# Kernel tuning notes

Hardware: AMD Instinct MI355X
Metric: run time of the kernel (lower is better)

The kernel has to match this reference:

```python
import jax, jax.numpy as jnp
import numpy as np

DIM = 1024
HEAD_DIM = 64
NUM_HEADS = DIM // HEAD_DIM
SCALE = HEAD_DIM ** -0.5
B, N, M = 2, 1024, 2048


def setup_inputs() -> dict:
    key = jax.random.key(0)
    ks = jax.random.split(key, 7)
    x = jax.random.normal(ks[0], (B, N, DIM), dtype=jnp.float32)
    context = jax.random.normal(ks[1], (B, M, DIM), dtype=jnp.float32)
    # query row has at least one valid key (avoids all -inf softmax rows).
    mask = jax.random.bernoulli(ks[2], 0.9, (B, N, M))
    mask = mask.at[:, :, 0].set(True)
    # Linear params (torch nn.Linear convention: y = x @ W.T + b)
    sq = (1.0 / DIM) ** 0.5
    Wq = jax.random.uniform(ks[3], (DIM, DIM), minval=-sq, maxval=sq, dtype=jnp.float32)
    Wkv = jax.random.uniform(ks[4], (2 * DIM, DIM), minval=-sq, maxval=sq, dtype=jnp.float32)
    b_kv = jax.random.uniform(ks[5], (2 * DIM,), minval=-sq, maxval=sq, dtype=jnp.float32)
    Wo = jax.random.uniform(ks[6], (DIM, DIM), minval=-sq, maxval=sq, dtype=jnp.float32)
    return {"x": x, "context": context, "mask": mask,
            "Wq": Wq, "Wkv": Wkv, "b_kv": b_kv, "Wo": Wo}


def reference(x, context, mask, Wq, Wkv, b_kv, Wo):
    b, n, c = x.shape
    m = context.shape[1]
    h, d = NUM_HEADS, HEAD_DIM
    # Q projection (no bias): [b, n, h, d] -> bhnd
    q = (x @ Wq.T).reshape(b, n, h, d).transpose(0, 2, 1, 3)
    # KV projection (with bias): [b, m, 2, h, d]
    kv = (context @ Wkv.T + b_kv).reshape(b, m, 2, h, d)
    k = kv[:, :, 0].transpose(0, 2, 1, 3)  # bhmd
    v = kv[:, :, 1].transpose(0, 2, 1, 3)  # bhmd
    # scores: bhnm, scale applied after matmul as in the original
    attn = jnp.einsum('bhnd,bhmd->bhnm', q, k) * SCALE
    attn = jnp.where(mask[:, None, :, :], attn, -jnp.inf)
    attn = jax.nn.softmax(attn, axis=-1)
    out = jnp.einsum('bhnm,bhmd->bhnd', attn, v)
    out = out.transpose(0, 2, 1, 3).reshape(b, n, h * d)
    return out @ Wo.T
```

## Files before the change

### kernel.cpp

```cpp
#include <hip/hip_runtime.h>


typedef __attribute__((ext_vector_type(8))) short short8;
typedef __attribute__((ext_vector_type(4))) short short4v;
typedef __attribute__((ext_vector_type(4))) float f32x4;

#define SCL2E 0.18033688011112042592f

__device__ __forceinline__ float bf2f(short s) {
  unsigned u = ((unsigned)(unsigned short)s) << 16;
  return __uint_as_float(u);
}
__device__ __forceinline__ short f2bf(float f) {
  unsigned u = __float_as_uint(f);
  u += 0x7fffu + ((u >> 16) & 1u);
  return (short)(u >> 16);
}
__device__ __forceinline__ void gld_lds16(const void* gp, void* lp) {
  __builtin_amdgcn_global_load_lds(
      (const __attribute__((address_space(1))) unsigned int*)gp,
      (__attribute__((address_space(3))) unsigned int*)lp, 16, 0, 0);
}
__device__ __forceinline__ short4v cvt4(float4 v) {
  short4v o;
  o[0] = f2bf(v.x); o[1] = f2bf(v.y); o[2] = f2bf(v.z); o[3] = f2bf(v.w);
  return o;
}
__device__ __forceinline__ size_t off128(int row, int k) {
  return ((size_t)(((row >> 7) * 32 + (k >> 5)) * 8 + ((row >> 4) & 7)) << 9) +
         (((((k >> 3) & 3) * 16 + (row & 15)) << 3) + (k & 7));
}
__device__ __forceinline__ size_t off64(int row, int k) {
  return ((size_t)(((row >> 6) * 32 + (k >> 5)) * 4 + ((row >> 4) & 3)) << 9) +
         (((((k >> 3) & 3) * 16 + (row & 15)) << 3) + (k & 7));
}

__global__ __launch_bounds__(256) void prep(
    const unsigned char* __restrict__ mask, unsigned long long* __restrict__ pm,
    const float* __restrict__ Wq, const float* __restrict__ Wkv,
    const float* __restrict__ Wo, const float* __restrict__ x,
    const float* __restrict__ ctx, short* __restrict__ wqb,
    short* __restrict__ wkvb, short* __restrict__ wob,
    short* __restrict__ xb, short* __restrict__ ctxb) {
  const int row = blockIdx.x;
  const int wave = threadIdx.x >> 6, lane = threadIdx.x & 63;
  const unsigned char p8 = mask[lane * 4 + 1];
  const int p32 = ((const int*)mask)[lane * 2 + 1];
  const int shift =
      (__ballot(p8 != 0) != 0ull) ? 0 : ((__ballot(p32 != 0) != 0ull) ? 2 : 3);
  const size_t mbase = ((size_t)row * 2048) << shift;
#pragma unroll
  for (int j = 0; j < 8; j++) {
    const int c = wave * 512 + j * 64 + lane;
    const unsigned long long bits = __ballot(mask[mbase + ((size_t)c << shift)] != 0);
    if (lane == 0) pm[(size_t)row * 32 + wave * 8 + j] = bits;
  }
  const int gid = blockIdx.x * 256 + threadIdx.x;
  {
    const int e = gid * 4, r = e >> 10, k = e & 1023;
    *(short4v*)(xb + off128(r, k)) = cvt4(((const float4*)x)[gid]);
  }
  {
    int e = gid * 4, r = e >> 10, k = e & 1023;
    *(short4v*)(ctxb + off128(r, k)) = cvt4(((const float4*)ctx)[gid]);
    e = (gid + 524288) * 4; r = e >> 10; k = e & 1023;
    *(short4v*)(ctxb + off128(r, k)) = cvt4(((const float4*)ctx)[gid + 524288]);
  }
  {
    const int e = gid * 4, r = e >> 10, k = e & 1023;
    *(short4v*)(wkvb + off128(r, k)) = cvt4(((const float4*)Wkv)[gid]);
  }
  if (gid < 262144) {
    const int e = gid * 4, r = e >> 10, k = e & 1023;
    *(short4v*)(wqb + off128(r, k)) = cvt4(((const float4*)Wq)[gid]);
    *(short4v*)(wob + off64(r, k)) = cvt4(((const float4*)Wo)[gid]);
  }
}

__global__ __launch_bounds__(256, 2)
void qkv_gemm(const short* __restrict__ xb, const short* __restrict__ ctxb,
              const short* __restrict__ wqb, const short* __restrict__ wkvb,
              const float* __restrict__ bias, short* __restrict__ qws,
              short* __restrict__ kws, short* __restrict__ vtws) {
  __shared__ __align__(16) short ldsA[8 * 512];
  __shared__ __align__(16) short ldsB[8 * 512];
  const int tid = threadIdx.x;
  const int wave = tid >> 6, lane = tid & 63;
  const int l15 = lane & 15, lg = lane >> 4;
  const int bx = blockIdx.x;
  const bool isKV = bx < 512;
  const int rt = isKV ? (bx >> 4) : ((bx - 512) >> 3);
  const int ct = isKV ? (bx & 15) : ((bx - 512) & 7);
  const short* Amat = isKV ? ctxb : xb;
  const short* Bw = isKV ? wkvb : wqb;
  const int wr = wave >> 1, wc = wave & 1;

  f32x4 acc[4][4];
#pragma unroll
  for (int i = 0; i < 4; i++)
#pragma unroll
    for (int j = 0; j < 4; j++) acc[i][j] = (f32x4){0.f, 0.f, 0.f, 0.f};

  const short* ga0 = Amat + (size_t)rt * 131072 + wave * 512 + lane * 8;
  const short* ga1 = ga0 + 2048;
  const short* gb0 = Bw + (size_t)ct * 131072 + wave * 512 + lane * 8;
  const short* gb1 = gb0 + 2048;
  short* la0 = &ldsA[wave * 512];
  short* la1 = &ldsA[(wave + 4) * 512];
  short* lb0 = &ldsB[wave * 512];
  short* lb1 = &ldsB[(wave + 4) * 512];

  for (int k0 = 0; k0 < 1024; k0 += 32) {
    const size_t koff = (size_t)(k0 >> 5) * 4096;
    __syncthreads();
    gld_lds16(ga0 + koff, la0);
    gld_lds16(ga1 + koff, la1);
    gld_lds16(gb0 + koff, lb0);
    gld_lds16(gb1 + koff, lb1);
    __syncthreads();
    short8 af[4], bfr[4];
#pragma unroll
    for (int t = 0; t < 4; t++)
      af[t] = *(const short8*)&ldsA[((wr * 4 + t) * 64 + lane) * 8];
#pragma unroll
    for (int t = 0; t < 4; t++)
      bfr[t] = *(const short8*)&ldsB[((wc * 4 + t) * 64 + lane) * 8];
#pragma unroll
    for (int i = 0; i < 4; i++)
#pragma unroll
      for (int j = 0; j < 4; j++)
        acc[i][j] =
            __builtin_amdgcn_mfma_f32_16x16x32_bf16(af[i], bfr[j], acc[i][j], 0, 0, 0);
  }

#pragma unroll
  for (int i = 0; i < 4; i++)
#pragma unroll
    for (int j = 0; j < 4; j++)
#pragma unroll
      for (int r = 0; r < 4; r++) {
        const int gr = rt * 128 + wr * 64 + i * 16 + lg * 4 + r;
        const int gc = ct * 128 + wc * 64 + j * 16 + l15;
        float v = acc[i][j][r];
        if (isKV) {
          v += bias[gc];
          const int b = gr >> 11, m = gr & 2047;
          const int kv = gc >> 10, hh = (gc >> 6) & 15, d = gc & 63;
          if (kv == 0)
            kws[((((size_t)b * 16 + hh) * 2048 + m) << 6) + d] = f2bf(v);
          else
            vtws[(((size_t)b * 16 + hh) * 64 + d) * 2048 + m] = f2bf(v);
        } else {
          const int b = gr >> 10, n = gr & 1023, hh = gc >> 6, d = gc & 63;
          qws[((((size_t)b * 16 + hh) * 1024 + n) << 6) + d] = f2bf(v * SCL2E);
        }
      }
}

__global__ __launch_bounds__(512, 2)
void attn_split(const short* __restrict__ Qg, const short* __restrict__ Kg,
                const short* __restrict__ Vtg,
                const unsigned int* __restrict__ pm,
                float* __restrict__ opart, float* __restrict__ lpart) {
  __shared__ __align__(16) short ldsK[8192];
  __shared__ __align__(16) short ldsV[8192];
  __shared__ __align__(16) short ldsP[17408];
  __shared__ __align__(16) short ones[512];
  const int tid = threadIdx.x;
  const int w = tid >> 6, lane = tid & 63;
  const int l15 = lane & 15, lg = lane >> 4;
  const int bx = blockIdx.x;
  const int bhid = bx & 31, qt = (bx >> 5) & 7, half = bx >> 8;
  const int b = bhid >> 4, h = bhid & 15;
  const int n0 = qt * 128, m_base = half * 1024;
  const size_t bh = (size_t)b * 16 + h;
  const short* Qb = Qg + (bh * 1024 + n0) * 64;
  const short* Kb = Kg + (bh << 17);
  const short* Vb = Vtg + (bh << 17);
  const unsigned int* pmw =
      pm + ((size_t)(b * 1024 + n0 + w * 16 + lg * 4) << 6) + (m_base >> 5);

  ones[tid] = 0x3F80;
#pragma unroll
  for (int ii = 0; ii < 2; ii++)
    gld_lds16(Qb + (size_t)(w * 16 + l15) * 64 + ii * 32 + lg * 8,
              &ldsP[(w * 2 + ii) * 512]);
  __syncthreads();
  short8 qf[2];
#pragma unroll
  for (int ks = 0; ks < 2; ks++)
    qf[ks] = *(const short8*)&ldsP[((w * 2 + ks) * 64 + lane) * 8];
  const short8 onesf = *(const short8*)&ones[lane * 8];

  f32x4 o[4], lacc;
#pragma unroll
  for (int ct = 0; ct < 4; ct++) o[ct] = (f32x4){0.f, 0.f, 0.f, 0.f};
  lacc = (f32x4){0.f, 0.f, 0.f, 0.f};
  short* Pme = &ldsP[w * 2176];

  uint4 mk[4], mkn[4];
#pragma unroll
  for (int r = 0; r < 4; r++) mk[r] = *(const uint4*)(pmw + (size_t)r * 64);

  for (int c = 0; c < 8; c++) {
    const int m0 = m_base + c * 128;
    __syncthreads();
#pragma unroll
    for (int ii = 0; ii < 2; ii++) {
      const int f = w * 2 + ii;
      const int t = f >> 1, ks = f & 1;
      gld_lds16(Kb + (size_t)(m0 + t * 16 + l15) * 64 + ks * 32 + lg * 8,
                &ldsK[f * 512]);
      const int ct = f >> 2, ks2 = f & 3;
      gld_lds16(Vb + (size_t)(ct * 16 + l15) * 2048 + (m0 + ks2 * 32 + lg * 8),
                &ldsV[f * 512]);
    }
    if (c < 7) {
#pragma unroll
      for (int r = 0; r < 4; r++)
        mkn[r] = *(const uint4*)(pmw + (size_t)r * 64 + (c + 1) * 4);
    }
    __syncthreads();

    f32x4 s[8];
#pragma unroll
    for (int t = 0; t < 8; t++) s[t] = (f32x4){0.f, 0.f, 0.f, 0.f};
#pragma unroll
    for (int t = 0; t < 8; t++)
#pragma unroll
      for (int ks = 0; ks < 2; ks++) {
        short8 kf = *(const short8*)&ldsK[((t * 2 + ks) * 64 + lane) * 8];
        s[t] = __builtin_amdgcn_mfma_f32_16x16x32_bf16(qf[ks], kf, s[t], 0, 0, 0);
      }

#pragma unroll
    for (int r = 0; r < 4; r++) {
      const unsigned int* mwp = (const unsigned int*)&mk[r];
#pragma unroll
      for (int t = 0; t < 8; t++) {
        const bool att = (mwp[t >> 1] >> (((t & 1) << 4) + l15)) & 1;
        const float p = exp2f(att ? s[t][r] : -1e30f);
        Pme[(lg * 4 + r) * 136 + t * 16 + l15] = f2bf(p);
      }
    }
    short8 pf[4];
#pragma unroll
    for (int ks2 = 0; ks2 < 4; ks2++)
      pf[ks2] = *(const short8*)&Pme[l15 * 136 + ks2 * 32 + lg * 8];
#pragma unroll
    for (int ct = 0; ct < 4; ct++)
#pragma unroll
      for (int ks2 = 0; ks2 < 4; ks2++) {
        short8 vf = *(const short8*)&ldsV[((ct * 4 + ks2) * 64 + lane) * 8];
        o[ct] = __builtin_amdgcn_mfma_f32_16x16x32_bf16(pf[ks2], vf, o[ct], 0, 0, 0);
      }
#pragma unroll
    for (int ks2 = 0; ks2 < 4; ks2++)
      lacc = __builtin_amdgcn_mfma_f32_16x16x32_bf16(pf[ks2], onesf, lacc, 0, 0, 0);
#pragma unroll
    for (int r = 0; r < 4; r++) mk[r] = mkn[r];
  }

#pragma unroll
  for (int ct = 0; ct < 4; ct++)
#pragma unroll
    for (int r = 0; r < 4; r++) {
      const int n = n0 + w * 16 + lg * 4 + r;
      opart[((size_t)half << 21) + (((size_t)b * 1024 + n) << 10) + h * 64 +
            ct * 16 + l15] = o[ct][r];
    }
  if (l15 == 0) {
#pragma unroll
    for (int r = 0; r < 4; r++) {
      const int n = n0 + w * 16 + lg * 4 + r;
      lpart[((size_t)half << 15) + bh * 1024 + n] = lacc[r];
    }
  }
}

__global__ __launch_bounds__(256) void combine(
    const float* __restrict__ opart, const float* __restrict__ lpart,
    short* __restrict__ aoT) {
  const int gid = blockIdx.x * 256 + threadIdx.x;
  const size_t base = (size_t)gid * 4;
  const int row = (int)(base >> 10), col = (int)(base & 1023);
  const int b = row >> 10, n = row & 1023, h = col >> 6;
  const float4 o1 = *(const float4*)(opart + base);
  const float4 o2 = *(const float4*)(opart + (1u << 21) + base);
  const float l1 = lpart[(size_t)(b * 16 + h) * 1024 + n];
  const float l2 = lpart[(1u << 15) + (size_t)(b * 16 + h) * 1024 + n];
  const float inv = 1.f / fmaxf(l1 + l2, 1e-30f);
  short4v o;
  o[0] = f2bf((o1.x + o2.x) * inv); o[1] = f2bf((o1.y + o2.y) * inv);
  o[2] = f2bf((o1.z + o2.z) * inv); o[3] = f2bf((o1.w + o2.w) * inv);
  *(short4v*)(aoT + off64(row, col)) = o;
}

__global__ __launch_bounds__(256, 2)
void o_gemm(const short* __restrict__ aoT, const short* __restrict__ wobT,
            float* __restrict__ Of) {
  __shared__ __align__(16) short ldsA[4 * 512];
  __shared__ __align__(16) short ldsB[4 * 512];
  const int tid = threadIdx.x;
  const int w = tid >> 6, lane = tid & 63;
  const int l15 = lane & 15, lg = lane >> 4;
  const int bx = blockIdx.x;
  const int rt = bx >> 4, ct = bx & 15;

  f32x4 acc[4];
#pragma unroll
  for (int j = 0; j < 4; j++) acc[j] = (f32x4){0.f, 0.f, 0.f, 0.f};

  const short* ga = aoT + (size_t)rt * 65536 + w * 512 + lane * 8;
  const short* gb = wobT + (size_t)ct * 65536 + w * 512 + lane * 8;
  short* la = &ldsA[w * 512];
  short* lb = &ldsB[w * 512];

  for (int k0 = 0; k0 < 1024; k0 += 32) {
    const size_t koff = (size_t)(k0 >> 5) * 2048;
    __syncthreads();
    gld_lds16(ga + koff, la);
    gld_lds16(gb + koff, lb);
    __syncthreads();
    const short8 af = *(const short8*)&ldsA[(w * 64 + lane) * 8];
#pragma unroll
    for (int j = 0; j < 4; j++) {
      const short8 bf = *(const short8*)&ldsB[(j * 64 + lane) * 8];
      acc[j] = __builtin_amdgcn_mfma_f32_16x16x32_bf16(af, bf, acc[j], 0, 0, 0);
    }
  }

#pragma unroll
  for (int j = 0; j < 4; j++)
#pragma unroll
    for (int r = 0; r < 4; r++) {
      const int gr = rt * 64 + w * 16 + lg * 4 + r;
      const int gc = ct * 64 + j * 16 + l15;
      Of[(size_t)gr * 1024 + gc] = acc[j][r];
    }
}

extern "C" void kernel_launch(void* const* d_in, const int* in_sizes, int n_in,
                              void* d_out, int out_size, void* d_ws, size_t ws_size,
                              hipStream_t stream) {
  const float* x   = (const float*)d_in[0];
  const float* ctx = (const float*)d_in[1];
  const unsigned char* mask = (const unsigned char*)d_in[2];
  const float* Wq  = (const float*)d_in[3];
  const float* Wkv = (const float*)d_in[4];
  const float* bkv = (const float*)d_in[5];
  const float* Wo  = (const float*)d_in[6];
  float* out = (float*)d_out;

  char* wsb = (char*)d_ws;
  short* qws  = (short*)(wsb);
  short* kws  = (short*)(wsb + (4u << 20));
  short* vtws = (short*)(wsb + (12u << 20));
  short* wqb  = (short*)(wsb + (20u << 20));
  short* wkvb = (short*)(wsb + (22u << 20));
  short* wob  = (short*)(wsb + (26u << 20));
  unsigned long long* pmws = (unsigned long long*)(wsb + (28u << 20));
  float* opart = (float*)(wsb + (29u << 20));
  float* lpart = (float*)(wsb + (45u << 20));
  short* xb   = (short*)(wsb + (29u << 20));
  short* ctxb = (short*)(wsb + (33u << 20));
  short* ao = (short*)(wsb + (20u << 20));

  prep<<<2048, 256, 0, stream>>>(mask, pmws, Wq, Wkv, Wo, x, ctx,
                                 wqb, wkvb, wob, xb, ctxb);
  qkv_gemm<<<640, 256, 0, stream>>>(xb, ctxb, wqb, wkvb, bkv, qws, kws, vtws);
  attn_split<<<512, 512, 0, stream>>>(qws, kws, vtws, (const unsigned int*)pmws,
                                      opart, lpart);
  combine<<<2048, 256, 0, stream>>>(opart, lpart, ao);
  o_gemm<<<512, 256, 0, stream>>>(ao, wob, out);
}
```

Measured before the change: 236.0 us.

## Keep softmax probabilities in registers via transposed QK^T and permuted V layout

Computes S^T (K as A operand) so each lane's accumulator rows line up with the bf16 A-fragment layout needed for the PV MFMA, and permutes the V^T workspace columns in the projection epilogue to match. This removes the LDS round trip for P and the ones buffer, cutting LDS use and allowing launch bounds of 6 blocks per CU. Probabilities are packed with v_cvt_pk_bf16_f32, and mask words are now loaded per chunk inside the loop rather than prefetched. The risks are correctness of the permutation mapping, and register pressure under the higher occupancy target.

```diff
diff --git a/kernel.cpp b/kernel.cpp
--- a/kernel.cpp
+++ b/kernel.cpp
@@ -4,6 +4,7 @@
 typedef __attribute__((ext_vector_type(8))) short short8;
 typedef __attribute__((ext_vector_type(4))) short short4v;
 typedef __attribute__((ext_vector_type(4))) float f32x4;
+typedef __attribute__((ext_vector_type(4))) int int4v;
 
 #define SCL2E 0.18033688011112042592f
 
@@ -15,6 +16,11 @@
   unsigned u = __float_as_uint(f);
   u += 0x7fffu + ((u >> 16) & 1u);
   return (short)(u >> 16);
+}
+__device__ __forceinline__ int cvt_pk_bf16(float a, float b) {
+  int r;
+  asm("v_cvt_pk_bf16_f32 %0, %1, %2" : "=v"(r) : "v"(a), "v"(b));
+  return r;
 }
 __device__ __forceinline__ void gld_lds16(const void* gp, void* lp) {
   __builtin_amdgcn_global_load_lds(
@@ -148,8 +154,11 @@
           const int kv = gc >> 10, hh = (gc >> 6) & 15, d = gc & 63;
           if (kv == 0)
             kws[((((size_t)b * 16 + hh) * 2048 + m) << 6) + d] = f2bf(v);
-          else
-            vtws[(((size_t)b * 16 + hh) * 64 + d) * 2048 + m] = f2bf(v);
+          else {
+            const int mp = (m & ~31) | (((m >> 2) & 3) << 3) |
+                           (((m >> 4) & 1) << 2) | (m & 3);
+            vtws[(((size_t)b * 16 + hh) * 64 + d) * 2048 + mp] = f2bf(v);
+          }
         } else {
           const int b = gr >> 10, n = gr & 1023, hh = gc >> 6, d = gc & 63;
           qws[((((size_t)b * 16 + hh) * 1024 + n) << 6) + d] = f2bf(v * SCL2E);
@@ -157,15 +166,13 @@
       }
 }
 
-__global__ __launch_bounds__(512, 2)
+__global__ __launch_bounds__(512, 6)
 void attn_split(const short* __restrict__ Qg, const short* __restrict__ Kg,
                 const short* __restrict__ Vtg,
                 const unsigned int* __restrict__ pm,
                 float* __restrict__ opart, float* __restrict__ lpart) {
   __shared__ __align__(16) short ldsK[8192];
   __shared__ __align__(16) short ldsV[8192];
-  __shared__ __align__(16) short ldsP[17408];
-  __shared__ __align__(16) short ones[512];
   const int tid = threadIdx.x;
   const int w = tid >> 6, lane = tid & 63;
   const int l15 = lane & 15, lg = lane >> 4;
@@ -178,32 +185,31 @@
   const short* Kb = Kg + (bh << 17);
   const short* Vb = Vtg + (bh << 17);
   const unsigned int* pmw =
-      pm + ((size_t)(b * 1024 + n0 + w * 16 + lg * 4) << 6) + (m_base >> 5);
-
-  ones[tid] = 0x3F80;
+      pm + ((size_t)(b * 1024 + n0 + w * 16 + l15) << 6) + (m_base >> 5);
+
 #pragma unroll
   for (int ii = 0; ii < 2; ii++)
     gld_lds16(Qb + (size_t)(w * 16 + l15) * 64 + ii * 32 + lg * 8,
-              &ldsP[(w * 2 + ii) * 512]);
+              &ldsK[(w * 2 + ii) * 512]);
   __syncthreads();
   short8 qf[2];
 #pragma unroll
   for (int ks = 0; ks < 2; ks++)
-    qf[ks] = *(const short8*)&ldsP[((w * 2 + ks) * 64 + lane) * 8];
-  const short8 onesf = *(const short8*)&ones[lane * 8];
+    qf[ks] = *(const short8*)&ldsK[((w * 2 + ks) * 64 + lane) * 8];
+
+  short8 onesf;
+#pragma unroll
+  for (int i = 0; i < 8; i++) onesf[i] = (short)0x3F80;
 
   f32x4 o[4], lacc;
 #pragma unroll
   for (int ct = 0; ct < 4; ct++) o[ct] = (f32x4){0.f, 0.f, 0.f, 0.f};
   lacc = (f32x4){0.f, 0.f, 0.f, 0.f};
-  short* Pme = &ldsP[w * 2176];
-
-  uint4 mk[4], mkn[4];
-#pragma unroll
-  for (int r = 0; r < 4; r++) mk[r] = *(const uint4*)(pmw + (size_t)r * 64);
+  const int sb = lg * 4;
 
   for (int c = 0; c < 8; c++) {
     const int m0 = m_base + c * 128;
+    const uint4 mk = *(const uint4*)(pmw + c * 4);
     __syncthreads();
 #pragma unroll
     for (int ii = 0; ii < 2; ii++) {
@@ -211,54 +217,54 @@
       const int t = f >> 1, ks = f & 1;
       gld_lds16(Kb + (size_t)(m0 + t * 16 + l15) * 64 + ks * 32 + lg * 8,
                 &ldsK[f * 512]);
-      const int ct = f >> 2, ks2 = f & 3;
-      gld_lds16(Vb + (size_t)(ct * 16 + l15) * 2048 + (m0 + ks2 * 32 + lg * 8),
+      const int vt = f >> 2, vk = f & 3;
+      gld_lds16(Vb + (size_t)(vt * 16 + l15) * 2048 + (m0 + vk * 32 + lg * 8),
                 &ldsV[f * 512]);
     }
-    if (c < 7) {
-#pragma unroll
-      for (int r = 0; r < 4; r++)
-        mkn[r] = *(const uint4*)(pmw + (size_t)r * 64 + (c + 1) * 4);
-    }
-    __syncthreads();
-
-    f32x4 s[8];
-#pragma unroll
-    for (int t = 0; t < 8; t++) s[t] = (f32x4){0.f, 0.f, 0.f, 0.f};
-#pragma unroll
-    for (int t = 0; t < 8; t++)
-#pragma unroll
-      for (int ks = 0; ks < 2; ks++) {
-        short8 kf = *(const short8*)&ldsK[((t * 2 + ks) * 64 + lane) * 8];
-        s[t] = __builtin_amdgcn_mfma_f32_16x16x32_bf16(qf[ks], kf, s[t], 0, 0, 0);
+    __syncthreads();
+
+    int4v pw4[4];
+#pragma unroll
+    for (int h2 = 0; h2 < 2; h2++) {
+      f32x4 s[4];
+#pragma unroll
+      for (int t2 = 0; t2 < 4; t2++) s[t2] = (f32x4){0.f, 0.f, 0.f, 0.f};
+#pragma unroll
+      for (int t2 = 0; t2 < 4; t2++) {
+        const int t = h2 * 4 + t2;
+#pragma unroll
+        for (int ks = 0; ks < 2; ks++) {
+          const short8 kf = *(const short8*)&ldsK[((t * 2 + ks) * 64 + lane) * 8];
+          s[t2] = __builtin_amdgcn_mfma_f32_16x16x32_bf16(kf, qf[ks], s[t2], 0, 0, 0);
+        }
       }
-
-#pragma unroll
-    for (int r = 0; r < 4; r++) {
-      const unsigned int* mwp = (const unsigned int*)&mk[r];
-#pragma unroll
-      for (int t = 0; t < 8; t++) {
-        const bool att = (mwp[t >> 1] >> (((t & 1) << 4) + l15)) & 1;
-        const float p = exp2f(att ? s[t][r] : -1e30f);
-        Pme[(lg * 4 + r) * 136 + t * 16 + l15] = f2bf(p);
+#pragma unroll
+      for (int t2 = 0; t2 < 4; t2++) {
+        const int t = h2 * 4 + t2;
+        const unsigned int mw = ((t >> 1) == 0) ? mk.x
+                              : ((t >> 1) == 1) ? mk.y
+                              : ((t >> 1) == 2) ? mk.z : mk.w;
+        float p[4];
+#pragma unroll
+        for (int r = 0; r < 4; r++) {
+          const bool att = (mw >> (((t & 1) << 4) + sb + r)) & 1;
+          p[r] = exp2f(att ? s[t2][r] : -1e30f);
+        }
+        pw4[t >> 1][(t & 1) * 2] = cvt_pk_bf16(p[0], p[1]);
+        pw4[t >> 1][(t & 1) * 2 + 1] = cvt_pk_bf16(p[2], p[3]);
       }
     }
-    short8 pf[4];
-#pragma unroll
-    for (int ks2 = 0; ks2 < 4; ks2++)
-      pf[ks2] = *(const short8*)&Pme[l15 * 136 + ks2 * 32 + lg * 8];
-#pragma unroll
-    for (int ct = 0; ct < 4; ct++)
-#pragma unroll
-      for (int ks2 = 0; ks2 < 4; ks2++) {
-        short8 vf = *(const short8*)&ldsV[((ct * 4 + ks2) * 64 + lane) * 8];
-        o[ct] = __builtin_amdgcn_mfma_f32_16x16x32_bf16(pf[ks2], vf, o[ct], 0, 0, 0);
+
+#pragma unroll
+    for (int ks2 = 0; ks2 < 4; ks2++) {
+      const short8 pf = __builtin_bit_cast(short8, pw4[ks2]);
+#pragma unroll
+      for (int ct = 0; ct < 4; ct++) {
+        const short8 vf = *(const short8*)&ldsV[((ct * 4 + ks2) * 64 + lane) * 8];
+        o[ct] = __builtin_amdgcn_mfma_f32_16x16x32_bf16(pf, vf, o[ct], 0, 0, 0);
       }
-#pragma unroll
-    for (int ks2 = 0; ks2 < 4; ks2++)
-      lacc = __builtin_amdgcn_mfma_f32_16x16x32_bf16(pf[ks2], onesf, lacc, 0, 0, 0);
-#pragma unroll
-    for (int r = 0; r < 4; r++) mk[r] = mkn[r];
+      lacc = __builtin_amdgcn_mfma_f32_16x16x32_bf16(pf, onesf, lacc, 0, 0, 0);
+    }
   }
 
 #pragma unroll
```

Result: no change. 232.9 us (-1.3%).
